# Kernel tuning notes

Measured on AMD Instinct MI355X. Metric: run time of the kernel, lower is better.

The kernel has to match this reference:

```python
import jax, jax.numpy as jnp
import numpy as np

B, NORB, N_UP, N_DN, HIDDEN = 1024, 128, 32, 32, 4096


def setup_inputs() -> dict:
    rng = np.random.default_rng(0)
    # Build valid occupancy configs: exactly N_UP up-electrons (bit 0) and
    # N_DN down-electrons (bit 1) per sample. Encoding: 0=empty,1=up,2=dn,3=updn.
    up_order = np.argsort(rng.random((B, NORB)), axis=1)
    dn_order = np.argsort(rng.random((B, NORB)), axis=1)
    up_bit = np.zeros((B, NORB), np.int32)
    dn_bit = np.zeros((B, NORB), np.int32)
    np.put_along_axis(up_bit, up_order[:, :N_UP], 1, axis=1)
    np.put_along_axis(dn_bit, dn_order[:, :N_DN], 1, axis=1)
    x = jnp.asarray(up_bit + 2 * dn_bit, dtype=jnp.int32)

    key = jax.random.key(0)
    k1, k2, k3 = jax.random.split(key, 3)
    orbitals = jax.random.normal(k1, (NORB, N_UP), jnp.float32)
    W1 = jax.random.normal(k2, (4 * NORB, HIDDEN), jnp.float32) / np.sqrt(4 * NORB)
    b1 = jnp.zeros((HIDDEN,), jnp.float32)
    W2 = jax.random.normal(k3, (HIDDEN, NORB * N_UP), jnp.float32) / np.sqrt(HIDDEN)
    b2 = jnp.zeros((NORB * N_UP,), jnp.float32)
    return {"x": x, "orbitals": orbitals, "W1": W1, "b1": b1, "W2": W2, "b2": b2}


def _occupancies_to_electrons(x, n_up, n_dn):
    # Per-spin sorted positions of occupied orbitals. Stable argsort on the
    # inverted mask keeps occupied sites first, in ascending orbital order.
    up_mask = (x & 1) == 1
    dn_mask = (x & 2) == 2
    y_up = jnp.argsort(jnp.where(up_mask, 0, 1), axis=-1, stable=True)[:, :n_up]
    y_dn = jnp.argsort(jnp.where(dn_mask, 0, 1), axis=-1, stable=True)[:, :n_dn]
    return y_up, y_dn


def reference(x, orbitals, W1, b1, W2, b2):
    Bsz, norb = x.shape
    n_up = orbitals.shape[1]

    # correction_fun: MLP on one-hot config -> [B, norb, n_up]
    h = jax.nn.one_hot(x, 4, dtype=W1.dtype).reshape(Bsz, -1)  # [B, 4*norb]
    h = jax.nn.relu(h @ W1 + b1)                               # [B, hidden]
    corrections = (h @ W2 + b2).reshape(Bsz, norb, n_up)       # [B, norb, n_up]

    y_up, y_dn = _occupancies_to_electrons(x, n_up, n_up)
    y_up = y_up[..., None]  # [B, n_up, 1]
    y_dn = y_dn[..., None]

    # gather orbital rows + correction rows per electron (spin-symmetric orbitals)
    phi_up = jnp.take_along_axis(orbitals[None], y_up, axis=1)  # [B, n_up, n_up]
    phi_dn = jnp.take_along_axis(orbitals[None], y_dn, axis=1)
    d_up = jnp.take_along_axis(corrections, y_up, axis=1)
    d_dn = jnp.take_along_axis(corrections, y_dn, axis=1)

    s_up, log_det_up = jnp.linalg.slogdet(phi_up + d_up)
    s_dn, log_det_dn = jnp.linalg.slogdet(phi_dn + d_dn)
    return log_det_up + log_det_dn + jnp.log(s_up * s_dn + 0j)  # complex [B]
```

## Files before the change

kernel.cpp:

```cpp
#include <hip/hip_runtime.h>
#include <cmath>

#define B_SZ  1024
#define NORB  128
#define NUP   32
#define HID   4096
#define NCORR (NORB * NUP)
#define K1    (4 * NORB)

typedef short  bf16x8 __attribute__((ext_vector_type(8)));
typedef float  f32x4  __attribute__((ext_vector_type(4)));

__device__ __forceinline__ unsigned short f2bf_rne(float f) {
    unsigned int u = __float_as_uint(f);
    u += 0x7FFFu + ((u >> 16) & 1u);
    return (unsigned short)(u >> 16);
}

__global__ __launch_bounds__(256) void k_packx(const int* __restrict__ x,
                                               unsigned int* __restrict__ xp) {
    int t = threadIdx.x;
    int row = blockIdx.x * 32 + (t >> 3);
    int d = t & 7;
    const int* src = x + row * NORB + d * 16;
    unsigned int dw = 0;
#pragma unroll
    for (int b = 0; b < 16; ++b) dw |= ((unsigned int)(src[b] & 3)) << (2 * b);
    xp[row * 8 + d] = dw;
}

__global__ __launch_bounds__(256) void k_splitW(const float* __restrict__ W,
                                                unsigned short* __restrict__ Bph,
                                                unsigned short* __restrict__ Bpl,
                                                int ktTot) {
    __shared__ float tile[64][33];
    int n0 = blockIdx.x * 32, k0 = blockIdx.y * 64;
    int t = threadIdx.x;
    int nl = t & 31, kg = t >> 5;
#pragma unroll
    for (int i = 0; i < 8; ++i) {
        int kl = kg + i * 8;
        tile[kl][nl] = W[(size_t)(k0 + kl) * 4096 + n0 + nl];
    }
    __syncthreads();

    int nt = (n0 + nl) >> 4;
    int kt = (k0 >> 5) + (kg >> 2);
    int lane_o = (kg & 3) * 16 + (nl & 15);
    size_t o = (((size_t)nt * ktTot + kt) * 64 + lane_o) * 8;

    unsigned short hi8[8], lo8[8];
#pragma unroll
    for (int j = 0; j < 8; ++j) {
        float v = tile[kg * 8 + j][nl];
        unsigned short hi = f2bf_rne(v);
        float fhi = __uint_as_float((unsigned int)hi << 16);
        hi8[j] = hi;
        lo8[j] = f2bf_rne(v - fhi);
    }
    *(bf16x8*)(Bph + o) = *(bf16x8*)hi8;
    *(bf16x8*)(Bpl + o) = *(bf16x8*)lo8;
}

__global__ __launch_bounds__(256) void k_hidden2(const unsigned int* __restrict__ xp,
                                                 const unsigned short* __restrict__ Bph,
                                                 const unsigned short* __restrict__ Bpl,
                                                 const float* __restrict__ b1,
                                                 unsigned short* __restrict__ h_hi,
                                                 unsigned short* __restrict__ h_lo) {
    __shared__ unsigned int sxp[64][8];
    __shared__ float Ht[64][132];

    int n0 = blockIdx.x * 128;
    int m0 = blockIdx.y * 64;
    int t = threadIdx.x;
    int w = t >> 6, lane = t & 63;
    int lm = lane & 15, kq = lane >> 4;
    int wn = w * 32;

#pragma unroll
    for (int i = 0; i < 2; ++i) {
        int idx = t + 256 * i;
        sxp[idx >> 3][idx & 7] = xp[(m0 + (idx >> 3)) * 8 + (idx & 7)];
    }
    __syncthreads();

    size_t nt0 = (size_t)((n0 + wn) >> 4);
    const unsigned short* bph = Bph + nt0 * (16 * 512) + (size_t)lane * 8;
    const unsigned short* bpl = Bpl + nt0 * (16 * 512) + (size_t)lane * 8;

    f32x4 acc[4][2] = {};

    bf16x8 nbh0 = *(const bf16x8*)(bph);
    bf16x8 nbh1 = *(const bf16x8*)(bph + 16 * 512);
    bf16x8 nbl0 = *(const bf16x8*)(bpl);
    bf16x8 nbl1 = *(const bf16x8*)(bpl + 16 * 512);

    for (int kt = 0; kt < 16; ++kt) {
        bf16x8 bh0 = nbh0, bh1 = nbh1, bl0 = nbl0, bl1 = nbl1;
        if (kt + 1 < 16) {
            nbh0 = *(const bf16x8*)(bph + (kt + 1) * 512);
            nbh1 = *(const bf16x8*)(bph + 16 * 512 + (kt + 1) * 512);
            nbl0 = *(const bf16x8*)(bpl + (kt + 1) * 512);
            nbl1 = *(const bf16x8*)(bpl + 16 * 512 + (kt + 1) * 512);
        }

        int i0 = kt * 8 + kq * 2;
        int dwIdx = i0 >> 4;
        int sh = (i0 & 15) * 2;
        bf16x8 af[4];
#pragma unroll
        for (int fm = 0; fm < 4; ++fm) {
            unsigned int dw = sxp[fm * 16 + lm][dwIdx];
            unsigned int c01 = (dw >> sh) & 0xFu;
            union { bf16x8 v; unsigned long long u[2]; } a;
            a.u[0] = 0x3F80ULL << ((c01 & 3u) * 16);
            a.u[1] = 0x3F80ULL << ((c01 >> 2) * 16);
            af[fm] = a.v;
        }

#pragma unroll
        for (int fm = 0; fm < 4; ++fm) {
            acc[fm][0] = __builtin_amdgcn_mfma_f32_16x16x32_bf16(af[fm], bh0, acc[fm][0], 0, 0, 0);
            acc[fm][0] = __builtin_amdgcn_mfma_f32_16x16x32_bf16(af[fm], bl0, acc[fm][0], 0, 0, 0);
            acc[fm][1] = __builtin_amdgcn_mfma_f32_16x16x32_bf16(af[fm], bh1, acc[fm][1], 0, 0, 0);
            acc[fm][1] = __builtin_amdgcn_mfma_f32_16x16x32_bf16(af[fm], bl1, acc[fm][1], 0, 0, 0);
        }
    }

#pragma unroll
    for (int fm = 0; fm < 4; ++fm)
#pragma unroll
        for (int fn = 0; fn < 2; ++fn) {
            int n = wn + fn * 16 + lm;
            float bv = b1[n0 + n];
#pragma unroll
            for (int r = 0; r < 4; ++r)
                Ht[fm * 16 + kq * 4 + r][n] = fmaxf(acc[fm][fn][r] + bv, 0.f);
        }
    __syncthreads();

    size_t mt0 = (size_t)(m0 >> 4), kt0 = (size_t)(n0 >> 5);
#pragma unroll
    for (int fi = 0; fi < 4; ++fi) {
        int f = w * 4 + fi;
        int mt = f >> 2, ktn = f & 3;
        int m = mt * 16 + lm;
        int kn = ktn * 32 + kq * 8;
        float4 v0 = *(const float4*)&Ht[m][kn];
        float4 v1 = *(const float4*)&Ht[m][kn + 4];
        float vv[8] = {v0.x, v0.y, v0.z, v0.w, v1.x, v1.y, v1.z, v1.w};
        unsigned short hi8[8], lo8[8];
#pragma unroll
        for (int j = 0; j < 8; ++j) {
            unsigned short hi = f2bf_rne(vv[j]);
            float fhi = __uint_as_float((unsigned int)hi << 16);
            hi8[j] = hi;
            lo8[j] = f2bf_rne(vv[j] - fhi);
        }
        size_t o = (((mt0 + mt) * 128 + (kt0 + ktn)) * 64 + lane) * 8;
        *(bf16x8*)(h_hi + o) = *(bf16x8*)hi8;
        *(bf16x8*)(h_lo + o) = *(bf16x8*)lo8;
    }
}

__global__ __launch_bounds__(256) void k_hidden_f32(const int* __restrict__ x,
                                                    const float* __restrict__ W1,
                                                    const float* __restrict__ b1,
                                                    float* __restrict__ h) {
    int b = blockIdx.x, tid = threadIdx.x;
    __shared__ int sx[NORB];
    if (tid < NORB) sx[tid] = x[b * NORB + tid];
    __syncthreads();
    float acc[16];
#pragma unroll
    for (int u = 0; u < 16; ++u) acc[u] = b1[tid + 256 * u];
    for (int i = 0; i < NORB; ++i) {
        const float* row = W1 + (size_t)(4 * i + sx[i]) * HID;
#pragma unroll
        for (int u = 0; u < 16; ++u) acc[u] += row[tid + 256 * u];
    }
    float* hb = h + (size_t)b * HID;
#pragma unroll
    for (int u = 0; u < 16; ++u) hb[tid + 256 * u] = fmaxf(acc[u], 0.f);
}

__global__ __launch_bounds__(256) void k_gemm4(const unsigned short* __restrict__ Ahp,
                                               const unsigned short* __restrict__ Alp,
                                               const unsigned short* __restrict__ Bph,
                                               const unsigned short* __restrict__ Bpl,
                                               const float* __restrict__ bias,
                                               float* __restrict__ C) {
    int n0 = blockIdx.x * 128;
    int m0 = blockIdx.y * 64;
    int t = threadIdx.x;
    int w = t >> 6, lane = t & 63;
    int lm = lane & 15, kq = lane >> 4;
    int wn = w * 32;

    size_t mt0 = (size_t)(m0 >> 4);
    size_t nt0 = (size_t)((n0 + wn) >> 4);
    const unsigned short* ah = Ahp + (mt0 * 128 * 64 + lane) * 8;
    const unsigned short* al = Alp + (mt0 * 128 * 64 + lane) * 8;
    const unsigned short* bh = Bph + (nt0 * 128 * 64 + lane) * 8;
    const unsigned short* bl = Bpl + (nt0 * 128 * 64 + lane) * 8;

    f32x4 acc[4][2] = {};
    bf16x8 cah[4], cal[4], cbh[2], cbl[2];

#pragma unroll
    for (int i = 0; i < 4; ++i) {
        cah[i] = *(const bf16x8*)(ah + (size_t)i * 65536);
        cal[i] = *(const bf16x8*)(al + (size_t)i * 65536);
    }
#pragma unroll
    for (int i = 0; i < 2; ++i) {
        cbh[i] = *(const bf16x8*)(bh + (size_t)i * 65536);
        cbl[i] = *(const bf16x8*)(bl + (size_t)i * 65536);
    }

    for (int kt = 0; kt < 128; ++kt) {
        int ktn = (kt + 1 < 128) ? kt + 1 : 127;
        bf16x8 nah[4], nal[4], nbh[2], nbl[2];
#pragma unroll
        for (int i = 0; i < 4; ++i) {
            nah[i] = *(const bf16x8*)(ah + (size_t)i * 65536 + (size_t)ktn * 512);
            nal[i] = *(const bf16x8*)(al + (size_t)i * 65536 + (size_t)ktn * 512);
        }
#pragma unroll
        for (int i = 0; i < 2; ++i) {
            nbh[i] = *(const bf16x8*)(bh + (size_t)i * 65536 + (size_t)ktn * 512);
            nbl[i] = *(const bf16x8*)(bl + (size_t)i * 65536 + (size_t)ktn * 512);
        }

#pragma unroll
        for (int fm = 0; fm < 4; ++fm) {
            acc[fm][0] = __builtin_amdgcn_mfma_f32_16x16x32_bf16(cah[fm], cbh[0], acc[fm][0], 0, 0, 0);
            acc[fm][0] = __builtin_amdgcn_mfma_f32_16x16x32_bf16(cal[fm], cbh[0], acc[fm][0], 0, 0, 0);
            acc[fm][0] = __builtin_amdgcn_mfma_f32_16x16x32_bf16(cah[fm], cbl[0], acc[fm][0], 0, 0, 0);
            acc[fm][1] = __builtin_amdgcn_mfma_f32_16x16x32_bf16(cah[fm], cbh[1], acc[fm][1], 0, 0, 0);
            acc[fm][1] = __builtin_amdgcn_mfma_f32_16x16x32_bf16(cal[fm], cbh[1], acc[fm][1], 0, 0, 0);
            acc[fm][1] = __builtin_amdgcn_mfma_f32_16x16x32_bf16(cah[fm], cbl[1], acc[fm][1], 0, 0, 0);
        }

#pragma unroll
        for (int i = 0; i < 4; ++i) { cah[i] = nah[i]; cal[i] = nal[i]; }
#pragma unroll
        for (int i = 0; i < 2; ++i) { cbh[i] = nbh[i]; cbl[i] = nbl[i]; }
    }

#pragma unroll
    for (int fm = 0; fm < 4; ++fm)
#pragma unroll
        for (int fn = 0; fn < 2; ++fn) {
            int n = n0 + wn + fn * 16 + lm;
            float bv = bias[n];
#pragma unroll
            for (int r = 0; r < 4; ++r) {
                int m = m0 + fm * 16 + kq * 4 + r;
                C[(size_t)m * NCORR + n] = acc[fm][fn][r] + bv;
            }
        }
}

#define BM 64
#define BN 64
#define BK 32
__global__ __launch_bounds__(256) void k_gemm(const float* __restrict__ A,
                                              const float* __restrict__ Bm,
                                              const float* __restrict__ bias,
                                              float* __restrict__ C) {
    __shared__ float As[BK][68];
    __shared__ float Bs[BK][BN];
    int n0 = blockIdx.x * BN, m0 = blockIdx.y * BM;
    int tid = threadIdx.x;
    int tm = tid >> 4, tn = tid & 15;
    int am = tid >> 3, ak = (tid & 7) * 4;
    int bk = tid >> 4, bn = (tid & 15) * 4;
    float acc[4][4] = {};
    for (int k0 = 0; k0 < HID; k0 += BK) {
#pragma unroll
        for (int s = 0; s < 2; ++s) {
            int m = am + 32 * s;
            float4 v = *(const float4*)(A + (size_t)(m0 + m) * HID + k0 + ak);
            As[ak + 0][m] = v.x; As[ak + 1][m] = v.y;
            As[ak + 2][m] = v.z; As[ak + 3][m] = v.w;
        }
#pragma unroll
        for (int s = 0; s < 2; ++s) {
            int k = bk + 16 * s;
            float4 v = *(const float4*)(Bm + (size_t)(k0 + k) * NCORR + n0 + bn);
            *(float4*)&Bs[k][bn] = v;
        }
        __syncthreads();
#pragma unroll
        for (int kk = 0; kk < BK; ++kk) {
            float4 a = *(const float4*)&As[kk][tm * 4];
            float4 bv = *(const float4*)&Bs[kk][tn * 4];
            float av[4] = {a.x, a.y, a.z, a.w};
            float bb[4] = {bv.x, bv.y, bv.z, bv.w};
#pragma unroll
            for (int i = 0; i < 4; ++i)
#pragma unroll
                for (int j = 0; j < 4; ++j) acc[i][j] += av[i] * bb[j];
        }
        __syncthreads();
    }
#pragma unroll
    for (int i = 0; i < 4; ++i) {
        int m = m0 + tm * 4 + i;
        float4 o;
        o.x = acc[i][0] + bias[n0 + tn * 4 + 0];
        o.y = acc[i][1] + bias[n0 + tn * 4 + 1];
        o.z = acc[i][2] + bias[n0 + tn * 4 + 2];
        o.w = acc[i][3] + bias[n0 + tn * 4 + 3];
        *(float4*)(C + (size_t)m * NCORR + n0 + tn * 4) = o;
    }
}

__global__ __launch_bounds__(128) void k_det(const int* __restrict__ x,
                                             const float* __restrict__ orbitals,
                                             const float* __restrict__ corr,
                                             float* __restrict__ out,
                                             int imag_off) {
    int b = blockIdx.x, tid = threadIdx.x;
    __shared__ int sx[NORB];
    __shared__ int yup[NUP], ydn[NUP];
    __shared__ float M[2][NUP][NUP + 1];
    __shared__ float rlog[2];
    __shared__ int rneg[2];

    sx[tid] = x[b * NORB + tid];
    __syncthreads();

    int occ = sx[tid];
    if (occ & 1) {
        int r = 0;
        for (int i = 0; i < tid; ++i) r += sx[i] & 1;
        yup[r] = tid;
    }
    if (occ & 2) {
        int r = 0;
        for (int i = 0; i < tid; ++i) r += (sx[i] >> 1) & 1;
        ydn[r] = tid;
    }
    __syncthreads();

    const float* cb = corr + (size_t)b * NCORR;
    for (int idx = tid; idx < 2 * NUP * NUP; idx += 128) {
        int s = idx >> 10;
        int i = (idx >> 5) & 31;
        int j = idx & 31;
        int r = s ? ydn[i] : yup[i];
        M[s][i][j] = orbitals[r * NUP + j] + cb[r * NUP + j];
    }
    __syncthreads();

    int wv = tid >> 6, lane = tid & 63;
    float (*Mm)[NUP + 1] = M[wv];
    float logdet = 0.f;
    int neg = 0;

    for (int k = 0; k < NUP; ++k) {
        float v = (lane >= k && lane < NUP) ? fabsf(Mm[lane][k]) : -1.f;
        int pi = lane;
#pragma unroll
        for (int off = 32; off > 0; off >>= 1) {
            float v2 = __shfl_down(v, off);
            int p2 = __shfl_down(pi, off);
            if (v2 > v) { v = v2; pi = p2; }
        }
        int p = __shfl(pi, 0);

        if (p != k) {
            if (lane < NUP) {
                float t1 = Mm[k][lane];
                Mm[k][lane] = Mm[p][lane];
                Mm[p][lane] = t1;
            }
            neg ^= 1;
        }
        __syncthreads();

        float pv = Mm[k][k];
        logdet += logf(fabsf(pv));
        if (pv < 0.f) neg ^= 1;

        int row = k + 1 + (lane & 31);
        int half = lane >> 5;
        if (row < NUP) {
            float f = Mm[row][k] / pv;
            for (int j = k + 1 + half; j < NUP; j += 2)
                Mm[row][j] -= f * Mm[k][j];
        }
        __syncthreads();
    }

    if (lane == 0) { rlog[wv] = logdet; rneg[wv] = neg; }
    __syncthreads();
    if (tid == 0) {
        out[b] = rlog[0] + rlog[1];
        if (imag_off > 0)
            out[imag_off + b] =
                (rneg[0] ^ rneg[1]) ? 3.14159265358979323846f : 0.f;
    }
}

extern "C" void kernel_launch(void* const* d_in, const int* in_sizes, int n_in,
                              void* d_out, int out_size, void* d_ws, size_t ws_size,
                              hipStream_t stream) {
    const int*   x        = (const int*)d_in[0];
    const float* orbitals = (const float*)d_in[1];
    const float* W1       = (const float*)d_in[2];
    const float* b1       = (const float*)d_in[3];
    const float* W2       = (const float*)d_in[4];
    const float* b2       = (const float*)d_in[5];
    float* out = (float*)d_out;
    int imag_off = (out_size == 2 * B_SZ) ? B_SZ : 0;

    const size_t need = (size_t)96 * 1024 * 1024;
    if (ws_size >= need) {
        unsigned short* h_hi = (unsigned short*)d_ws;
        unsigned short* h_lo = h_hi + (size_t)B_SZ * HID;
        unsigned short* Bph  = h_lo + (size_t)B_SZ * HID;
        unsigned short* Bpl  = Bph + (size_t)HID * NCORR;
        float*          corr = (float*)(Bpl + (size_t)HID * NCORR);

        unsigned short* W1ph = (unsigned short*)corr;
        unsigned short* W1pl = W1ph + (size_t)K1 * HID;
        unsigned int*   xp   = (unsigned int*)(W1pl + (size_t)K1 * HID);

        k_packx<<<B_SZ / 32, 256, 0, stream>>>(x, xp);
        k_splitW<<<dim3(HID / 32, K1 / 64), 256, 0, stream>>>(W1, W1ph, W1pl, 16);
        k_splitW<<<dim3(NCORR / 32, HID / 64), 256, 0, stream>>>(W2, Bph, Bpl, 128);

        k_hidden2<<<dim3(HID / 128, B_SZ / 64), 256, 0, stream>>>(xp, W1ph, W1pl, b1, h_hi, h_lo);

        dim3 g2(NCORR / 128, B_SZ / 64);
        k_gemm4<<<g2, 256, 0, stream>>>(h_hi, h_lo, Bph, Bpl, b2, corr);
        k_det<<<B_SZ, 128, 0, stream>>>(x, orbitals, corr, out, imag_off);
    } else {
        float* h    = (float*)d_ws;
        float* corr = h + (size_t)B_SZ * HID;
        k_hidden_f32<<<B_SZ, 256, 0, stream>>>(x, W1, b1, h);
        dim3 g2(NCORR / BN, B_SZ / BM);
        k_gemm<<<g2, 256, 0, stream>>>(h, W2, b2, corr);
        k_det<<<B_SZ, 128, 0, stream>>>(x, orbitals, corr, out, imag_off);
    }
}
```

Measured before the change: 291.8 us.

## Share A fragments via LDS in GEMM, fuse x packing, vectorize W split loads

The main GEMM now has each wave load one A m-tile from global memory and stage it in shared memory, where all four waves read it. Previously every wave loaded all four A tiles itself, so this removes redundant global A traffic. It processes two k-steps per barrier and sets launch bounds to two blocks per CU. Separately, the k_packx kernel is folded into k_hidden2 to save a launch, and k_splitW reads W with float4 loads. The trade-off is added barriers and LDS usage, and the B operand is no longer prefetched across iterations, which may expose load latency.

```diff
diff --git a/kernel.cpp b/kernel.cpp
--- a/kernel.cpp
+++ b/kernel.cpp
@@ -15,18 +15,6 @@
     unsigned int u = __float_as_uint(f);
     u += 0x7FFFu + ((u >> 16) & 1u);
     return (unsigned short)(u >> 16);
-}
-
-__global__ __launch_bounds__(256) void k_packx(const int* __restrict__ x,
-                                               unsigned int* __restrict__ xp) {
-    int t = threadIdx.x;
-    int row = blockIdx.x * 32 + (t >> 3);
-    int d = t & 7;
-    const int* src = x + row * NORB + d * 16;
-    unsigned int dw = 0;
-#pragma unroll
-    for (int b = 0; b < 16; ++b) dw |= ((unsigned int)(src[b] & 3)) << (2 * b);
-    xp[row * 8 + d] = dw;
 }
 
 __global__ __launch_bounds__(256) void k_splitW(const float* __restrict__ W,
@@ -36,14 +24,18 @@
     __shared__ float tile[64][33];
     int n0 = blockIdx.x * 32, k0 = blockIdx.y * 64;
     int t = threadIdx.x;
+
+    int rl = t >> 3, c4 = (t & 7) * 4;
+#pragma unroll
+    for (int i = 0; i < 2; ++i) {
+        int kl = rl + 32 * i;
+        float4 v = *(const float4*)(W + (size_t)(k0 + kl) * 4096 + n0 + c4);
+        tile[kl][c4 + 0] = v.x; tile[kl][c4 + 1] = v.y;
+        tile[kl][c4 + 2] = v.z; tile[kl][c4 + 3] = v.w;
+    }
+    __syncthreads();
+
     int nl = t & 31, kg = t >> 5;
-#pragma unroll
-    for (int i = 0; i < 8; ++i) {
-        int kl = kg + i * 8;
-        tile[kl][nl] = W[(size_t)(k0 + kl) * 4096 + n0 + nl];
-    }
-    __syncthreads();
-
     int nt = (n0 + nl) >> 4;
     int kt = (k0 >> 5) + (kg >> 2);
     int lane_o = (kg & 3) * 16 + (nl & 15);
@@ -62,7 +54,7 @@
     *(bf16x8*)(Bpl + o) = *(bf16x8*)lo8;
 }
 
-__global__ __launch_bounds__(256) void k_hidden2(const unsigned int* __restrict__ xp,
+__global__ __launch_bounds__(256) void k_hidden2(const int* __restrict__ x,
                                                  const unsigned short* __restrict__ Bph,
                                                  const unsigned short* __restrict__ Bpl,
                                                  const float* __restrict__ b1,
@@ -80,8 +72,13 @@
 
 #pragma unroll
     for (int i = 0; i < 2; ++i) {
-        int idx = t + 256 * i;
-        sxp[idx >> 3][idx & 7] = xp[(m0 + (idx >> 3)) * 8 + (idx & 7)];
+        int id = t + 256 * i;
+        int row = id >> 3, d = id & 7;
+        const int* src = x + (size_t)(m0 + row) * NORB + d * 16;
+        unsigned int dw = 0;
+#pragma unroll
+        for (int b = 0; b < 16; ++b) dw |= ((unsigned int)(src[b] & 3)) << (2 * b);
+        sxp[row][d] = dw;
     }
     __syncthreads();
 
@@ -185,12 +182,14 @@
     for (int u = 0; u < 16; ++u) hb[tid + 256 * u] = fmaxf(acc[u], 0.f);
 }
 
-__global__ __launch_bounds__(256) void k_gemm4(const unsigned short* __restrict__ Ahp,
-                                               const unsigned short* __restrict__ Alp,
-                                               const unsigned short* __restrict__ Bph,
-                                               const unsigned short* __restrict__ Bpl,
-                                               const float* __restrict__ bias,
-                                               float* __restrict__ C) {
+__global__ __launch_bounds__(256, 2) void k_gemm6(const unsigned short* __restrict__ Ahp,
+                                                  const unsigned short* __restrict__ Alp,
+                                                  const unsigned short* __restrict__ Bph,
+                                                  const unsigned short* __restrict__ Bpl,
+                                                  const float* __restrict__ bias,
+                                                  float* __restrict__ C) {
+    __shared__ unsigned short AF[2][2][4][512];
+
     int n0 = blockIdx.x * 128;
     int m0 = blockIdx.y * 64;
     int t = threadIdx.x;
@@ -198,55 +197,78 @@
     int lm = lane & 15, kq = lane >> 4;
     int wn = w * 32;
 
-    size_t mt0 = (size_t)(m0 >> 4);
-    size_t nt0 = (size_t)((n0 + wn) >> 4);
-    const unsigned short* ah = Ahp + (mt0 * 128 * 64 + lane) * 8;
-    const unsigned short* al = Alp + (mt0 * 128 * 64 + lane) * 8;
-    const unsigned short* bh = Bph + (nt0 * 128 * 64 + lane) * 8;
-    const unsigned short* bl = Bpl + (nt0 * 128 * 64 + lane) * 8;
+    int mt0 = m0 >> 4;
+    int nt0 = (n0 + wn) >> 4;
+
+    const unsigned short* agh = Ahp + (size_t)(mt0 + w) * 65536 + (size_t)lane * 8;
+    const unsigned short* agl = Alp + (size_t)(mt0 + w) * 65536 + (size_t)lane * 8;
+    const unsigned short* bh0 = Bph + (size_t)nt0 * 65536 + (size_t)lane * 8;
+    const unsigned short* bh1 = Bph + (size_t)(nt0 + 1) * 65536 + (size_t)lane * 8;
+    const unsigned short* bl0 = Bpl + (size_t)nt0 * 65536 + (size_t)lane * 8;
+    const unsigned short* bl1 = Bpl + (size_t)(nt0 + 1) * 65536 + (size_t)lane * 8;
 
     f32x4 acc[4][2] = {};
-    bf16x8 cah[4], cal[4], cbh[2], cbl[2];
-
-#pragma unroll
-    for (int i = 0; i < 4; ++i) {
-        cah[i] = *(const bf16x8*)(ah + (size_t)i * 65536);
-        cal[i] = *(const bf16x8*)(al + (size_t)i * 65536);
-    }
-#pragma unroll
-    for (int i = 0; i < 2; ++i) {
-        cbh[i] = *(const bf16x8*)(bh + (size_t)i * 65536);
-        cbl[i] = *(const bf16x8*)(bl + (size_t)i * 65536);
-    }
-
-    for (int kt = 0; kt < 128; ++kt) {
-        int ktn = (kt + 1 < 128) ? kt + 1 : 127;
-        bf16x8 nah[4], nal[4], nbh[2], nbl[2];
-#pragma unroll
-        for (int i = 0; i < 4; ++i) {
-            nah[i] = *(const bf16x8*)(ah + (size_t)i * 65536 + (size_t)ktn * 512);
-            nal[i] = *(const bf16x8*)(al + (size_t)i * 65536 + (size_t)ktn * 512);
-        }
-#pragma unroll
-        for (int i = 0; i < 2; ++i) {
-            nbh[i] = *(const bf16x8*)(bh + (size_t)i * 65536 + (size_t)ktn * 512);
-            nbl[i] = *(const bf16x8*)(bl + (size_t)i * 65536 + (size_t)ktn * 512);
-        }
-
-#pragma unroll
-        for (int fm = 0; fm < 4; ++fm) {
-            acc[fm][0] = __builtin_amdgcn_mfma_f32_16x16x32_bf16(cah[fm], cbh[0], acc[fm][0], 0, 0, 0);
-            acc[fm][0] = __builtin_amdgcn_mfma_f32_16x16x32_bf16(cal[fm], cbh[0], acc[fm][0], 0, 0, 0);
-            acc[fm][0] = __builtin_amdgcn_mfma_f32_16x16x32_bf16(cah[fm], cbl[0], acc[fm][0], 0, 0, 0);
-            acc[fm][1] = __builtin_amdgcn_mfma_f32_16x16x32_bf16(cah[fm], cbh[1], acc[fm][1], 0, 0, 0);
-            acc[fm][1] = __builtin_amdgcn_mfma_f32_16x16x32_bf16(cal[fm], cbh[1], acc[fm][1], 0, 0, 0);
-            acc[fm][1] = __builtin_amdgcn_mfma_f32_16x16x32_bf16(cah[fm], cbl[1], acc[fm][1], 0, 0, 0);
-        }
-
-#pragma unroll
-        for (int i = 0; i < 4; ++i) { cah[i] = nah[i]; cal[i] = nal[i]; }
-#pragma unroll
-        for (int i = 0; i < 2; ++i) { cbh[i] = nbh[i]; cbl[i] = nbl[i]; }
+
+    float4 rh0 = *(const float4*)(agh);
+    float4 rh1 = *(const float4*)(agh + 512);
+    float4 rl0 = *(const float4*)(agl);
+    float4 rl1 = *(const float4*)(agl + 512);
+
+    for (int ktp = 0; ktp < 64; ++ktp) {
+        if (ktp) __syncthreads();
+
+        int o0 = (2 * ktp) * 512, o1 = o0 + 512;
+        bf16x8 B00h = *(const bf16x8*)(bh0 + o0);
+        bf16x8 B01h = *(const bf16x8*)(bh1 + o0);
+        bf16x8 B00l = *(const bf16x8*)(bl0 + o0);
+        bf16x8 B01l = *(const bf16x8*)(bl1 + o0);
+        bf16x8 B10h = *(const bf16x8*)(bh0 + o1);
+        bf16x8 B11h = *(const bf16x8*)(bh1 + o1);
+        bf16x8 B10l = *(const bf16x8*)(bl0 + o1);
+        bf16x8 B11l = *(const bf16x8*)(bl1 + o1);
+
+        *(float4*)&AF[0][0][w][lane * 8] = rh0;
+        *(float4*)&AF[1][0][w][lane * 8] = rh1;
+        *(float4*)&AF[0][1][w][lane * 8] = rl0;
+        *(float4*)&AF[1][1][w][lane * 8] = rl1;
+        __syncthreads();
+
+        int kn = (ktp + 1 < 64) ? ktp + 1 : 63;
+        rh0 = *(const float4*)(agh + (size_t)(2 * kn) * 512);
+        rh1 = *(const float4*)(agh + (size_t)(2 * kn + 1) * 512);
+        rl0 = *(const float4*)(agl + (size_t)(2 * kn) * 512);
+        rl1 = *(const float4*)(agl + (size_t)(2 * kn + 1) * 512);
+
+        bf16x8 ah[4], al[4];
+#pragma unroll
+        for (int fm = 0; fm < 4; ++fm) {
+            ah[fm] = *(const bf16x8*)&AF[0][0][fm][lane * 8];
+            al[fm] = *(const bf16x8*)&AF[0][1][fm][lane * 8];
+        }
+#pragma unroll
+        for (int fm = 0; fm < 4; ++fm) {
+            acc[fm][0] = __builtin_amdgcn_mfma_f32_16x16x32_bf16(ah[fm], B00h, acc[fm][0], 0, 0, 0);
+            acc[fm][0] = __builtin_amdgcn_mfma_f32_16x16x32_bf16(al[fm], B00h, acc[fm][0], 0, 0, 0);
+            acc[fm][0] = __builtin_amdgcn_mfma_f32_16x16x32_bf16(ah[fm], B00l, acc[fm][0], 0, 0, 0);
+            acc[fm][1] = __builtin_amdgcn_mfma_f32_16x16x32_bf16(ah[fm], B01h, acc[fm][1], 0, 0, 0);
+            acc[fm][1] = __builtin_amdgcn_mfma_f32_16x16x32_bf16(al[fm], B01h, acc[fm][1], 0, 0, 0);
+            acc[fm][1] = __builtin_amdgcn_mfma_f32_16x16x32_bf16(ah[fm], B01l, acc[fm][1], 0, 0, 0);
+        }
+
+#pragma unroll
+        for (int fm = 0; fm < 4; ++fm) {
+            ah[fm] = *(const bf16x8*)&AF[1][0][fm][lane * 8];
+            al[fm] = *(const bf16x8*)&AF[1][1][fm][lane * 8];
+        }
+#pragma unroll
+        for (int fm = 0; fm < 4; ++fm) {
+            acc[fm][0] = __builtin_amdgcn_mfma_f32_16x16x32_bf16(ah[fm], B10h, acc[fm][0], 0, 0, 0);
+            acc[fm][0] = __builtin_amdgcn_mfma_f32_16x16x32_bf16(al[fm], B10h, acc[fm][0], 0, 0, 0);
+            acc[fm][0] = __builtin_amdgcn_mfma_f32_16x16x32_bf16(ah[fm], B10l, acc[fm][0], 0, 0, 0);
+            acc[fm][1] = __builtin_amdgcn_mfma_f32_16x16x32_bf16(ah[fm], B11h, acc[fm][1], 0, 0, 0);
+            acc[fm][1] = __builtin_amdgcn_mfma_f32_16x16x32_bf16(al[fm], B11h, acc[fm][1], 0, 0, 0);
+            acc[fm][1] = __builtin_amdgcn_mfma_f32_16x16x32_bf16(ah[fm], B11l, acc[fm][1], 0, 0, 0);
+        }
     }
 
 #pragma unroll
@@ -428,16 +450,14 @@
 
         unsigned short* W1ph = (unsigned short*)corr;
         unsigned short* W1pl = W1ph + (size_t)K1 * HID;
-        unsigned int*   xp   = (unsigned int*)(W1pl + (size_t)K1 * HID);
-
-        k_packx<<<B_SZ / 32, 256, 0, stream>>>(x, xp);
+
         k_splitW<<<dim3(HID / 32, K1 / 64), 256, 0, stream>>>(W1, W1ph, W1pl, 16);
         k_splitW<<<dim3(NCORR / 32, HID / 64), 256, 0, stream>>>(W2, Bph, Bpl, 128);
 
-        k_hidden2<<<dim3(HID / 128, B_SZ / 64), 256, 0, stream>>>(xp, W1ph, W1pl, b1, h_hi, h_lo);
+        k_hidden2<<<dim3(HID / 128, B_SZ / 64), 256, 0, stream>>>(x, W1ph, W1pl, b1, h_hi, h_lo);
 
         dim3 g2(NCORR / 128, B_SZ / 64);
-        k_gemm4<<<g2, 256, 0, stream>>>(h_hi, h_lo, Bph, Bpl, b2, corr);
+        k_gemm6<<<g2, 256, 0, stream>>>(h_hi, h_lo, Bph, Bpl, b2, corr);
         k_det<<<B_SZ, 128, 0, stream>>>(x, orbitals, corr, out, imag_off);
     } else {
         float* h    = (float*)d_ws;
```

Measured after the change: 261.3 us. -10.5%, faster.
